# Optimization experiments

Measured on AMD Instinct MI355X. Metric: run time of the kernel, lower is better.

## Reference

```python
import jax, jax.numpy as jnp
import numpy as np

B, I, T, H, K = 64, 32, 1024, 512, 8  # K = number of extra pathways


def setup_inputs() -> dict:
    key = jax.random.key(0)
    ks = jax.random.split(key, 32)
    stdv = 1.0 / np.sqrt(H)
    u = lambda k, shp: jax.random.uniform(k, shp, jnp.float32, -stdv, stdv)
    inp = {}
    inp['Y'] = jax.random.normal(ks[0], (B, I, T), jnp.float32)
    for j in range(K):
        inp[f'x{j+1}'] = jax.random.normal(ks[1 + j], (B, 3, T), jnp.float32)
    # main gates
    inp['W_i'], inp['U_i'], inp['b_i'] = u(ks[9], (I, H)), u(ks[10], (H, H)), u(ks[11], (H,))
    inp['W_f'], inp['U_f'], inp['b_f'] = u(ks[12], (I, H)), u(ks[13], (H, H)), u(ks[14], (H,))
    inp['W_c'], inp['U_c'], inp['b_c'] = u(ks[15], (I, H)), u(ks[16], (H, H)), u(ks[17], (H,))
    inp['W_o'], inp['U_o'], inp['b_o'] = u(ks[18], (I, H)), u(ks[19], (H, H)), u(ks[20], (H,))
    # stacked extra pathways: [K,3,H], [K,H,H], [K,H]
    inp['W_i_x'] = u(ks[21], (K, 3, H))
    inp['U_i_x'] = u(ks[22], (K, H, H))
    inp['b_i_x'] = u(ks[23], (K, H))
    inp['W_c_x'] = u(ks[24], (K, 3, H))
    inp['U_c_x'] = u(ks[25], (K, H, H))
    inp['b_c_x'] = u(ks[26], (K, H))
    inp['W_a'], inp['b_a'] = u(ks[27], (H, H)), u(ks[28], (H,))
    return inp


def _forward(Y, x1, x2, x3, x4, x5, x6, x7, x8,
             W_i, U_i, b_i, W_f, U_f, b_f, W_c, U_c, b_c, W_o, U_o, b_o,
             W_i_x, U_i_x, b_i_x, W_c_x, U_c_x, b_c_x, W_a, b_a):
    xs = jnp.stack([x1, x2, x3, x4, x5, x6, x7, x8], axis=0)  # [K,B,3,T]
    # Original code quirk: input gates i_x3..i_x8 all consume x2_t.
    gate_idx = jnp.array([0, 1, 1, 1, 1, 1, 1, 1])
    xs_i = xs[gate_idx]                                        # [K,B,3,T]
    Y_T = jnp.transpose(Y, (2, 0, 1))        # [T,B,I]
    xsi_T = jnp.transpose(xs_i, (3, 1, 0, 2))  # [T,B,K,3]
    xsc_T = jnp.transpose(xs, (3, 1, 0, 2))    # [T,B,K,3]

    def step(carry, inp):
        h, c = carry
        Y_t, xi_t, xc_t = inp
        i_t = jax.nn.sigmoid(Y_t @ W_i + h @ U_i + b_i)                      # [B,H]
        i_x = jax.nn.sigmoid(jnp.einsum('bki,kih->bkh', xi_t, W_i_x)
                             + jnp.einsum('bh,kho->bko', h, U_i_x) + b_i_x)  # [B,K,H]
        f_t = jax.nn.sigmoid(Y_t @ W_f + h @ U_f + b_f)
        Ct = jnp.tanh(Y_t @ W_c + h @ U_c + b_c)
        Cx = jnp.tanh(jnp.einsum('bki,kih->bkh', xc_t, W_c_x)
                      + jnp.einsum('bh,kho->bko', h, U_c_x) + b_c_x)
        o_t = jax.nn.sigmoid(Y_t @ W_o + h @ U_o + b_o)
        l_all = jnp.concatenate([(Ct * i_t)[:, None, :], Cx * i_x], axis=1)  # [B,9,H]
        u_all = jnp.tanh(jnp.einsum('bkh,ho->bko', l_all, W_a) * c[:, None, :] + b_a)
        alpha = jax.nn.softmax(u_all, axis=1)
        L_t = jnp.sum(alpha * l_all, axis=1)                                 # [B,H]
        c = f_t * c + L_t
        h = o_t * jnp.tanh(c)
        return (h, c), h

    h0 = jnp.zeros((Y.shape[0], W_a.shape[0]), Y.dtype)
    (h_T, _), hs = jax.lax.scan(step, (h0, h0), (Y_T, xsi_T, xsc_T))
    hidden_seq = jnp.transpose(hs, (1, 0, 2))  # [B,T,H]
    return h_T, hidden_seq


def reference(Y, x1, x2, x3, x4, x5, x6, x7, x8,
              W_i, U_i, b_i, W_f, U_f, b_f, W_c, U_c, b_c, W_o, U_o, b_o,
              W_i_x, U_i_x, b_i_x, W_c_x, U_c_x, b_c_x, W_a, b_a):
    return _forward(Y, x1, x2, x3, x4, x5, x6, x7, x8,
                    W_i, U_i, b_i, W_f, U_f, b_f, W_c, U_c, b_c, W_o, U_o, b_o,
                    W_i_x, U_i_x, b_i_x, W_c_x, U_c_x, b_c_x, W_a, b_a)
```

## Files before the change

### kernel.cpp

```cpp
#include <hip/hip_runtime.h>
#include <hip/hip_bf16.h>

typedef __hip_bfloat16 bf16;
typedef unsigned long long u64;

#define NSTEP 1024
#define BATCH 64
#define HID   512
#define GRID  256
#define NTHR  512
#define KC    64

#define OFF_BAR   0u
#define OFF_FLAG  640u
#define OFF_HG    1024u
#define OFF_CG    132096u
#define OFF_GALL  263168u
#define OFF_UCAT  2884608u
#define OFF_WA    23856128u
#define OFF_WM    24904704u
#define OFF_WX    25166848u
#define OFF_BM    25265152u
#define OFF_BX    25273344u
#define OFF_BA    25306112u
#define OFF_YT    25308160u
#define OFF_XT    33696768u

#define L_US    0
#define L_WML   20960
#define L_HA    22400
#define L_YA    31104
#define L_XA    33216
#define L_RED   34752
#define L_GB    36224
#define L_LB    31104
#define L_RA    22400
#define L_RB    27264
#define L_MPZ   29696
#define L_TOT   39240

#define US(c,k)    smem[L_US  + (c)*524 + (k)]
#define WML(c,j)   smem[L_WML + (c)*36  + (j)]
#define HA(s,b,k)  smem[L_HA  + (s)*4352 + (b)*68 + (k)]
#define YA(b,j)    smem[L_YA  + (b)*33 + (j)]
#define XA(a,b,j)  smem[L_XA  + ((a)*64 + (b))*3 + (j)]
#define RED(q,j)   smem[L_RED + (q)*11 + (j)]
#define GB(r,c)    smem[L_GB  + (r)*40 + (c)]
#define LB(j,h)    smem[L_LB  + (j)*520 + (h)]

struct RawIn {
  const void *Y, *x[8];
  const void *W_i,*U_i,*b_i, *W_f,*U_f,*b_f, *W_c,*U_c,*b_c, *W_o,*U_o,*b_o;
  const void *W_ix,*U_ix,*b_ix, *W_cx,*U_cx,*b_cx, *W_a,*b_a;
  float *Ucat,*Wa,*Wm,*Wx,*Bm,*Bx,*Ba,*Yt,*Xt;
  const unsigned *flag;
};

struct Params {
  const float *Ucat,*Wa,*Wm,*Wx,*Bm,*Bx,*Ba,*Yt,*Xt;
  float *Hg,*Cg,*Gall;
  unsigned *bar;
  const unsigned *flag;
  void *out;
};

__global__ void k_detect(const unsigned short* __restrict__ p, unsigned* flag) {
  if (blockIdx.x == 0 && threadIdx.x == 0) {
    int cnt = 0;
    for (int i = 0; i < 64; ++i) {
      unsigned e = (p[i] >> 7) & 0xFF;
      cnt += (e >= 0x60 && e <= 0x7C) || (p[i] & 0x7FFF) == 0;
    }
    *flag = (cnt >= 56) ? 1u : 0u;
  }
}

__device__ __forceinline__ float cvt(const void* p, size_t i, bool bf) {
  return bf ? (float)((const bf16*)p)[i] : ((const float*)p)[i];
}

#define NWTOT 5605888
__global__ __launch_bounds__(256)
void k_conv_w(RawIn R) {
  const bool bf = (*R.flag) != 0;
  for (size_t i = blockIdx.x*256 + threadIdx.x; i < NWTOT; i += (size_t)gridDim.x*256) {
    if (i < 5242880) {
      size_t g = i >> 18, r = i & 262143;
      const void* s = g<4 ? (g==0?R.U_i:g==1?R.U_f:g==2?R.U_c:R.U_o)
                    : g<12 ? R.U_ix : R.U_cx;
      size_t off = g<4 ? r : g<12 ? (g-4)*262144 + r : (g-12)*262144 + r;
      R.Ucat[i] = cvt(s, off, bf);
    } else {
      size_t j = i - 5242880;
      if (j < 262144) { R.Wa[j] = cvt(R.W_a, j, bf); }
      else {
        size_t j2 = j - 262144;
        if (j2 < 65536) {
          size_t g = j2 >> 14, r = j2 & 16383;
          const void* s = g==0?R.W_i:g==1?R.W_f:g==2?R.W_c:R.W_o;
          R.Wm[j2] = cvt(s, r, bf);
        } else {
          size_t j3 = j2 - 65536;
          if (j3 < 24576) {
            size_t p = j3 / 1536, r = j3 % 1536;
            R.Wx[j3] = p < 8 ? cvt(R.W_ix, p*1536 + r, bf)
                             : cvt(R.W_cx, (p-8)*1536 + r, bf);
          } else {
            size_t j4 = j3 - 24576;
            if (j4 < 2048) {
              size_t g = j4 >> 9, c = j4 & 511;
              const void* s = g==0?R.b_i:g==1?R.b_f:g==2?R.b_c:R.b_o;
              R.Bm[j4] = cvt(s, c, bf);
            } else {
              size_t j5 = j4 - 2048;
              if (j5 < 8192) {
                size_t p = j5 >> 9, c = j5 & 511;
                R.Bx[j5] = p < 8 ? cvt(R.b_ix, p*512 + c, bf)
                                 : cvt(R.b_cx, (p-8)*512 + c, bf);
              } else {
                size_t j6 = j5 - 8192;
                R.Ba[j6] = cvt(R.b_a, j6, bf);
              }
            }
          }
        }
      }
    }
  }
}

#define NYT 2097152
#define NXT 1572864
__global__ __launch_bounds__(256)
void k_conv_in(RawIn R) {
  const bool bf = (*R.flag) != 0;
  for (size_t i = blockIdx.x*256 + threadIdx.x; i < NYT+NXT; i += (size_t)gridDim.x*256) {
    if (i < NYT) {
      size_t j = i & 31, b = (i >> 5) & 63, t = i >> 11;
      R.Yt[i] = cvt(R.Y, (b*32 + j)*NSTEP + t, bf);
    } else {
      size_t i2 = i - NYT;
      size_t j = i2 % 3, r = i2 / 3;
      size_t b = r & 63; r >>= 6;
      size_t a = r & 7, t = r >> 3;
      R.Xt[i2] = cvt(R.x[a], (b*3 + j)*NSTEP + t, bf);
    }
  }
}


__device__ __forceinline__ float sigf(float v){ return 1.f/(1.f+expf(-v)); }

__device__ __forceinline__ float gload(const float* p){
  return __hip_atomic_load(p, __ATOMIC_RELAXED, __HIP_MEMORY_SCOPE_AGENT);
}
__device__ __forceinline__ u64 gload2(const float* p){
  return __hip_atomic_load((const u64*)p, __ATOMIC_RELAXED, __HIP_MEMORY_SCOPE_AGENT);
}
__device__ __forceinline__ void gstore(float* p, float v){
  __hip_atomic_store(p, v, __ATOMIC_RELAXED, __HIP_MEMORY_SCOPE_AGENT);
}
__device__ __forceinline__ void gstore2(float* p, float x, float y){
  union { u64 u_; float f[2]; } v; v.f[0]=x; v.f[1]=y;
  __hip_atomic_store((u64*)p, v.u_, __ATOMIC_RELAXED, __HIP_MEMORY_SCOPE_AGENT);
}

__device__ __forceinline__ void gbar(unsigned* base, unsigned bi, int w) {
  asm volatile("s_waitcnt vmcnt(0)" ::: "memory");
  __syncthreads();
  if (threadIdx.x == 0) {
    unsigned* xcd  = base + 16 + 16*(w & 7);
    unsigned* glob = base;
    unsigned* rel  = base + 144;
    __hip_atomic_fetch_add(xcd, 1u, __ATOMIC_RELAXED, __HIP_MEMORY_SCOPE_AGENT);
    if (w < 8) {
      unsigned* mine = base + 16 + 16*w;
      while (__hip_atomic_load(mine, __ATOMIC_RELAXED, __HIP_MEMORY_SCOPE_AGENT) < bi*32u)
        __builtin_amdgcn_s_sleep(1);
      __hip_atomic_fetch_add(glob, 1u, __ATOMIC_RELAXED, __HIP_MEMORY_SCOPE_AGENT);
    }
    if (w == 0) {
      while (__hip_atomic_load(glob, __ATOMIC_RELAXED, __HIP_MEMORY_SCOPE_AGENT) < bi*8u)
        __builtin_amdgcn_s_sleep(1);
      __hip_atomic_store(rel, bi, __ATOMIC_RELAXED, __HIP_MEMORY_SCOPE_AGENT);
    } else {
      while (__hip_atomic_load(rel, __ATOMIC_RELAXED, __HIP_MEMORY_SCOPE_AGENT) < bi)
        __builtin_amdgcn_s_sleep(2);
    }
  }
  __syncthreads();
}


__global__ __launch_bounds__(NTHR, 2)
void lstm_main(Params P) {
  extern __shared__ float smem[];

  const bool bfout = (*P.flag) != 0;

  const int w   = blockIdx.x;
  const int tid = threadIdx.x;
  const int c0  = w * 40;
  const int cgr = tid & 7;
  const int rgr = (tid >> 3) & 31;
  const int ksl = tid >> 8;
  const int cl  = cgr * 5;
  const int pb  = w >> 2;
  const int ph0 = (w & 3) * 128;
  const int hg  = tid & 63;
  const int kq8 = tid >> 6;

  for (int e = tid; e < 40*512; e += NTHR) {
    int c = e >> 9, k = e & 511;
    int cg = c0 + c, g = cg >> 9, cc = cg & 511;
    US(c, k) = P.Ucat[((size_t)g*HID + k)*HID + cc];
  }
  for (int e = tid; e < 40*33; e += NTHR) {
    int c = e / 33, jj = e % 33;
    int cg = c0 + c, g = cg >> 9, cc = cg & 511;
    float v;
    if (jj == 32) {
      v = g < 4  ? P.Bm[g*HID + cc]
        : g < 12 ? P.Bx[(g-4)*HID + cc]
                 : P.Bx[(8 + g-12)*HID + cc];
    } else if (g < 4) {
      v = P.Wm[((size_t)g*32 + jj)*HID + cc];
    } else if (jj < 3) {
      int p = (g < 12) ? (g-4) : (8 + g-12);
      v = P.Wx[((size_t)p*3 + jj)*HID + cc];
    } else v = 0.f;
    WML(c, jj) = v;
  }
  __syncthreads();

  unsigned bi = 0;

  u64 pre[8];
  auto hgld = [&](int kcc) {
#pragma unroll
    for (int u = 0; u < 8; ++u) {
      int e2 = tid + u*NTHR;
      int s2 = e2 >> 11, b = (e2 >> 5) & 63, k = (e2 & 31) * 2;
      pre[u] = gload2(&P.Hg[(size_t)b*HID + s2*256 + kcc + k]);
    }
  };

  for (int t = 0; t < NSTEP; ++t) {
    for (int e = tid; e < 64*32; e += NTHR) {
      int b = e >> 5, j = e & 31;
      YA(b, j) = P.Yt[((size_t)t*BATCH + b)*32 + j];
    }
    for (int e = tid; e < 8*64*3; e += NTHR) {
      int j2 = e % 3; int r = e / 3; int b = r & 63; int a = r >> 6;
      XA(a, b, j2) = P.Xt[(((size_t)t*8 + a)*BATCH + b)*3 + j2];
    }

    hgld(0);

    float acc[2][5];
#pragma unroll
    for (int i=0;i<2;++i)
#pragma unroll
      for (int j=0;j<5;++j) acc[i][j]=0.f;

    for (int kc = 0; kc < 256; kc += KC) {
      __syncthreads();
#pragma unroll
      for (int u = 0; u < 8; ++u) {
        int e2 = tid + u*NTHR;
        int s2 = e2 >> 11, b = (e2 >> 5) & 63, k = (e2 & 31) * 2;
        union { u64 u_; float f[2]; } v; v.u_ = pre[u];
        float2 t2; t2.x = v.f[0]; t2.y = v.f[1];
        *(float2*)&HA(s2, b, k) = t2;
      }
      __syncthreads();
      if (kc + KC < 256) hgld(kc + KC);

      const int kb = ksl*256 + kc;
#pragma unroll 4
      for (int kk = 0; kk < KC; kk += 4) {
        float4 h0 = *(const float4*)&HA(ksl, rgr,      kk);
        float4 h1 = *(const float4*)&HA(ksl, rgr+32,   kk);
#pragma unroll
        for (int j = 0; j < 5; ++j) {
          float4 u = *(const float4*)&US(cl+j, kb+kk);
          acc[0][j] += h0.x*u.x; acc[0][j] += h0.y*u.y;
          acc[0][j] += h0.z*u.z; acc[0][j] += h0.w*u.w;
          acc[1][j] += h1.x*u.x; acc[1][j] += h1.y*u.y;
          acc[1][j] += h1.z*u.z; acc[1][j] += h1.w*u.w;
        }
      }
    }

    if (ksl) {
      int q = tid - 256;
#pragma unroll
      for (int i=0;i<2;++i)
#pragma unroll
        for (int j=0;j<5;++j) RED(q, i*5+j) = acc[i][j];
    }
    __syncthreads();

    float vv[2][5];
    if (!ksl) {
#pragma unroll
      for (int i = 0; i < 2; ++i) {
        int row = rgr + 32*i;
#pragma unroll
        for (int j = 0; j < 5; ++j) {
          int c = cl + j, cg = c0 + c, g = cg >> 9;
          float v = acc[i][j] + RED(tid, i*5+j);
          float s = WML(c, 32);
          if (g < 4) {
            for (int jj = 0; jj < 32; ++jj)
              s += YA(row, jj) * WML(c, jj);
            v += s;
            v = (g==2) ? tanhf(v) : sigf(v);
          } else if (g < 12) {
            int p = g-4; int a = (p==0) ? 0 : 1;
            for (int jj = 0; jj < 3; ++jj)
              s += XA(a, row, jj) * WML(c, jj);
            v = sigf(v + s);
          } else {
            int p = g-12;
            for (int jj = 0; jj < 3; ++jj)
              s += XA(p, row, jj) * WML(c, jj);
            v = tanhf(v + s);
          }
          vv[i][j] = v;
        }
      }
    }
    __syncthreads();
    if (!ksl) {
#pragma unroll
      for (int i = 0; i < 2; ++i)
#pragma unroll
        for (int j = 0; j < 5; ++j)
          GB(rgr + 32*i, cl + j) = vv[i][j];
    }
    __syncthreads();
    for (int e = tid; e < 64*20; e += NTHR) {
      int row = e / 20, p = e % 20;
      int cc2 = c0 + 2*p;
      int g = cc2 >> 9, cc = cc2 & 511;
      gstore2(&P.Gall[((size_t)g*BATCH + row)*HID + cc], GB(row, 2*p), GB(row, 2*p+1));
    }

    gbar(P.bar, ++bi, w);

    for (int e = tid; e < 9*256; e += NTHR) {
      int j = e >> 8, h2 = (e & 255) << 1;
      union { u64 u_; float f[2]; } a, b2;
      if (j == 0) {
        a.u_  = gload2(&P.Gall[((size_t)0*BATCH+pb)*HID+h2]);
        b2.u_ = gload2(&P.Gall[((size_t)2*BATCH+pb)*HID+h2]);
      } else {
        int p = j-1;
        a.u_  = gload2(&P.Gall[((size_t)(4+p)*BATCH+pb)*HID+h2]);
        b2.u_ = gload2(&P.Gall[((size_t)(12+p)*BATCH+pb)*HID+h2]);
      }
      float2 t2; t2.x = a.f[0]*b2.f[0]; t2.y = a.f[1]*b2.f[1];
      *(float2*)&LB(j, h2) = t2;
    }
    __syncthreads();

    float ab[2][9];
#pragma unroll
    for (int s=0;s<2;++s)
#pragma unroll
      for (int j=0;j<9;++j) ab[s][j]=0.f;
    {
      const int k0 = kq8 * 64;
      const float* wa = P.Wa + (size_t)k0*HID + ph0 + hg*2;
#pragma unroll 4
      for (int k = 0; k < 64; k += 4) {
        float2 w0 = *(const float2*)&wa[(size_t)(k+0)*HID];
        float2 w1 = *(const float2*)&wa[(size_t)(k+1)*HID];
        float2 w2 = *(const float2*)&wa[(size_t)(k+2)*HID];
        float2 w3 = *(const float2*)&wa[(size_t)(k+3)*HID];
#pragma unroll
        for (int j=0;j<9;++j) {
          float4 l4 = *(const float4*)&LB(j, k0+k);
          ab[0][j] += l4.x*w0.x; ab[0][j] += l4.y*w1.x;
          ab[0][j] += l4.z*w2.x; ab[0][j] += l4.w*w3.x;
          ab[1][j] += l4.x*w0.y; ab[1][j] += l4.y*w1.y;
          ab[1][j] += l4.z*w2.y; ab[1][j] += l4.w*w3.y;
        }
      }
    }
    if (tid >= 256) {
      float* r = &smem[L_RA + (tid-256)*19];
#pragma unroll
      for (int s=0;s<2;++s)
#pragma unroll
        for (int j=0;j<9;++j) r[s*9+j] = ab[s][j];
    }
    __syncthreads();
    if (tid < 256) {
      const float* r = &smem[L_RA + tid*19];
#pragma unroll
      for (int s=0;s<2;++s)
#pragma unroll
        for (int j=0;j<9;++j) ab[s][j] += r[s*9+j];
      if (tid >= 128) {
        float* r2 = &smem[L_RB + (tid-128)*19];
#pragma unroll
        for (int s=0;s<2;++s)
#pragma unroll
          for (int j=0;j<9;++j) r2[s*9+j] = ab[s][j];
      }
    }
    __syncthreads();
    if (tid < 128) {
      const float* r = &smem[L_RB + tid*19];
#pragma unroll
      for (int s=0;s<2;++s)
#pragma unroll
        for (int j=0;j<9;++j) ab[s][j] += r[s*9+j];
      if (tid >= 64) {
        float* r2 = &smem[L_RA + (tid-64)*19];
#pragma unroll
        for (int s=0;s<2;++s)
#pragma unroll
          for (int j=0;j<9;++j) r2[s*9+j] = ab[s][j];
      }
    }
    __syncthreads();
    if (tid < 64) {
      const float* r = &smem[L_RA + tid*19];
      float* mp = &smem[L_MPZ + tid*19];
#pragma unroll
      for (int s=0;s<2;++s)
#pragma unroll
        for (int j=0;j<9;++j) mp[s*9+j] = ab[s][j] + r[s*9+j];
    }
    __syncthreads();
    if (tid < 128) {
      const int hp = ph0 + tid;
      const float* mf = &smem[L_MPZ + (tid>>1)*19 + (tid&1)*9];
      float co = P.Cg[(size_t)pb*HID + hp];
      float ba = P.Ba[hp];
      float u9[9], mx = -1e30f;
#pragma unroll
      for (int j=0;j<9;++j) {
        u9[j] = tanhf(mf[j]*co + ba);
        mx = fmaxf(mx, u9[j]);
      }
      float ssum = 0.f, L = 0.f;
#pragma unroll
      for (int j=0;j<9;++j) {
        float e2 = expf(u9[j]-mx);
        ssum += e2;
        L += e2 * LB(j, hp);
      }
      L /= ssum;
      float f = gload(&P.Gall[((size_t)1*BATCH+pb)*HID + hp]);
      float o = gload(&P.Gall[((size_t)3*BATCH+pb)*HID + hp]);
      float cn = f*co + L;
      float hn = o*tanhf(cn);
      P.Cg[(size_t)pb*HID + hp] = cn;
      gstore(&P.Hg[(size_t)pb*HID + hp], hn);
      size_t iseq = (size_t)BATCH*HID + ((size_t)pb*NSTEP + t)*HID + hp;
      if (bfout) ((bf16*)P.out)[iseq] = __float2bfloat16(hn);
      else       ((float*)P.out)[iseq] = hn;
      if (t == NSTEP-1) {
        size_t ih = (size_t)pb*HID + hp;
        if (bfout) ((bf16*)P.out)[ih] = __float2bfloat16(hn);
        else       ((float*)P.out)[ih] = hn;
      }
    }

    gbar(P.bar, ++bi, w);
  }
}


extern "C" void kernel_launch(void* const* d_in, const int* in_sizes, int n_in,
                              void* d_out, int out_size, void* d_ws, size_t ws_size,
                              hipStream_t stream) {
  char* ws = (char*)d_ws;

  RawIn R;
  R.Y = d_in[0];
  for (int i = 0; i < 8; ++i) R.x[i] = d_in[1+i];
  R.W_i=d_in[9];  R.U_i=d_in[10]; R.b_i=d_in[11];
  R.W_f=d_in[12]; R.U_f=d_in[13]; R.b_f=d_in[14];
  R.W_c=d_in[15]; R.U_c=d_in[16]; R.b_c=d_in[17];
  R.W_o=d_in[18]; R.U_o=d_in[19]; R.b_o=d_in[20];
  R.W_ix=d_in[21]; R.U_ix=d_in[22]; R.b_ix=d_in[23];
  R.W_cx=d_in[24]; R.U_cx=d_in[25]; R.b_cx=d_in[26];
  R.W_a =d_in[27]; R.b_a =d_in[28];
  R.Ucat=(float*)(ws+OFF_UCAT); R.Wa=(float*)(ws+OFF_WA);
  R.Wm=(float*)(ws+OFF_WM); R.Wx=(float*)(ws+OFF_WX);
  R.Bm=(float*)(ws+OFF_BM); R.Bx=(float*)(ws+OFF_BX); R.Ba=(float*)(ws+OFF_BA);
  R.Yt=(float*)(ws+OFF_YT); R.Xt=(float*)(ws+OFF_XT);
  R.flag=(const unsigned*)(ws+OFF_FLAG);

  Params P;
  P.Ucat=R.Ucat; P.Wa=R.Wa; P.Wm=R.Wm; P.Wx=R.Wx;
  P.Bm=R.Bm; P.Bx=R.Bx; P.Ba=R.Ba; P.Yt=R.Yt; P.Xt=R.Xt;
  P.Hg=(float*)(ws+OFF_HG); P.Cg=(float*)(ws+OFF_CG); P.Gall=(float*)(ws+OFF_GALL);
  P.bar=(unsigned*)(ws+OFF_BAR);
  P.flag=R.flag;
  P.out=d_out;

  hipMemsetAsync(d_ws, 0, OFF_GALL, stream);

  k_detect<<<1, 64, 0, stream>>>((const unsigned short*)d_in[10], (unsigned*)(ws+OFF_FLAG));
  k_conv_w <<<21899, 256, 0, stream>>>(R);
  k_conv_in<<<14336, 256, 0, stream>>>(R);

  const int smemBytes = L_TOT * 4;
  hipFuncSetAttribute((const void*)lstm_main,
                      hipFuncAttributeMaxDynamicSharedMemorySize, smemBytes);
  lstm_main<<<dim3(GRID), dim3(NTHR), smemBytes, stream>>>(P);
}
```

Before: 51.85 ms.

## Split recurrent matmul into four K-slices with packed FMA and vectorized input projection

Restructures the per-step recurrent h·U product so each thread computes 4 batch rows × 5 columns over a quarter of K, instead of 2 rows over a half. The inner product uses v_pk_fma_f32 packed float2 FMAs, and the four partial sums are reduced through shared memory. The Y·W input projection is vectorized with float4 loads, with padded layouts to match. The aim is more register reuse of the U loads and higher FMA throughput per instruction. In exchange it uses more accumulator registers and adds a 4-way shared-memory reduction with an extra barrier.

```diff
diff --git a/kernel.cpp b/kernel.cpp
--- a/kernel.cpp
+++ b/kernel.cpp
@@ -9,7 +9,6 @@
 #define HID   512
 #define GRID  256
 #define NTHR  512
-#define KC    64
 
 #define OFF_BAR   0u
 #define OFF_FLAG  640u
@@ -29,22 +28,21 @@
 #define L_US    0
 #define L_WML   20960
 #define L_HA    22400
-#define L_YA    31104
-#define L_XA    33216
-#define L_RED   34752
-#define L_GB    36224
-#define L_LB    31104
+#define L_YA    31616
+#define L_XA    33920
+#define L_GB    35456
+#define L_REDA  22400
+#define L_LB    31616
 #define L_RA    22400
 #define L_RB    27264
 #define L_MPZ   29696
-#define L_TOT   39240
+#define L_TOT   38016
 
 #define US(c,k)    smem[L_US  + (c)*524 + (k)]
 #define WML(c,j)   smem[L_WML + (c)*36  + (j)]
-#define HA(s,b,k)  smem[L_HA  + (s)*4352 + (b)*68 + (k)]
-#define YA(b,j)    smem[L_YA  + (b)*33 + (j)]
+#define HA(q,b,k)  smem[L_HA  + (q)*2304 + (b)*36 + (k)]
+#define YA(b,j)    smem[L_YA  + (b)*36 + (j)]
 #define XA(a,b,j)  smem[L_XA  + ((a)*64 + (b))*3 + (j)]
-#define RED(q,j)   smem[L_RED + (q)*11 + (j)]
 #define GB(r,c)    smem[L_GB  + (r)*40 + (c)]
 #define LB(j,h)    smem[L_LB  + (j)*520 + (h)]
 
@@ -165,6 +163,10 @@
   __hip_atomic_store((u64*)p, v.u_, __ATOMIC_RELAXED, __HIP_MEMORY_SCOPE_AGENT);
 }
 
+__device__ __forceinline__ void pkfma(float2& d, float2 a, float2 b){
+  asm("v_pk_fma_f32 %0, %1, %2, %0" : "+v"(d) : "v"(a), "v"(b));
+}
+
 __device__ __forceinline__ void gbar(unsigned* base, unsigned bi, int w) {
   asm volatile("s_waitcnt vmcnt(0)" ::: "memory");
   __syncthreads();
@@ -202,8 +204,8 @@
   const int tid = threadIdx.x;
   const int c0  = w * 40;
   const int cgr = tid & 7;
-  const int rgr = (tid >> 3) & 31;
-  const int ksl = tid >> 8;
+  const int rgr = (tid >> 3) & 15;
+  const int ksl = tid >> 7;
   const int cl  = cgr * 5;
   const int pb  = w >> 2;
   const int ph0 = (w & 3) * 128;
@@ -215,20 +217,20 @@
     int cg = c0 + c, g = cg >> 9, cc = cg & 511;
     US(c, k) = P.Ucat[((size_t)g*HID + k)*HID + cc];
   }
-  for (int e = tid; e < 40*33; e += NTHR) {
-    int c = e / 33, jj = e % 33;
+  for (int e = tid; e < 40*36; e += NTHR) {
+    int c = e / 36, jj = e % 36;
     int cg = c0 + c, g = cg >> 9, cc = cg & 511;
-    float v;
+    float v = 0.f;
     if (jj == 32) {
       v = g < 4  ? P.Bm[g*HID + cc]
         : g < 12 ? P.Bx[(g-4)*HID + cc]
                  : P.Bx[(8 + g-12)*HID + cc];
-    } else if (g < 4) {
+    } else if (jj < 32 && g < 4) {
       v = P.Wm[((size_t)g*32 + jj)*HID + cc];
     } else if (jj < 3) {
       int p = (g < 12) ? (g-4) : (8 + g-12);
       v = P.Wx[((size_t)p*3 + jj)*HID + cc];
-    } else v = 0.f;
+    }
     WML(c, jj) = v;
   }
   __syncthreads();
@@ -240,8 +242,10 @@
 #pragma unroll
     for (int u = 0; u < 8; ++u) {
       int e2 = tid + u*NTHR;
-      int s2 = e2 >> 11, b = (e2 >> 5) & 63, k = (e2 & 31) * 2;
-      pre[u] = gload2(&P.Hg[(size_t)b*HID + s2*256 + kcc + k]);
+      int k  = (e2 & 15) * 2;
+      int b  = (e2 >> 4) & 63;
+      int q  = e2 >> 10;
+      pre[u] = gload2(&P.Hg[(size_t)b*HID + q*128 + kcc + k]);
     }
   };
 
@@ -257,87 +261,147 @@
 
     hgld(0);
 
-    float acc[2][5];
-#pragma unroll
-    for (int i=0;i<2;++i)
-#pragma unroll
-      for (int j=0;j<5;++j) acc[i][j]=0.f;
-
-    for (int kc = 0; kc < 256; kc += KC) {
+    float2 acc2[4][5];
+#pragma unroll
+    for (int i=0;i<4;++i)
+#pragma unroll
+      for (int j=0;j<5;++j) { acc2[i][j].x=0.f; acc2[i][j].y=0.f; }
+
+    for (int kc = 0; kc < 128; kc += 32) {
       __syncthreads();
 #pragma unroll
       for (int u = 0; u < 8; ++u) {
         int e2 = tid + u*NTHR;
-        int s2 = e2 >> 11, b = (e2 >> 5) & 63, k = (e2 & 31) * 2;
+        int k  = (e2 & 15) * 2;
+        int b  = (e2 >> 4) & 63;
+        int q  = e2 >> 10;
         union { u64 u_; float f[2]; } v; v.u_ = pre[u];
         float2 t2; t2.x = v.f[0]; t2.y = v.f[1];
-        *(float2*)&HA(s2, b, k) = t2;
+        *(float2*)&HA(q, b, k) = t2;
       }
       __syncthreads();
-      if (kc + KC < 256) hgld(kc + KC);
-
-      const int kb = ksl*256 + kc;
-#pragma unroll 4
-      for (int kk = 0; kk < KC; kk += 4) {
+      if (kc + 32 < 128) hgld(kc + 32);
+
+      const int kbase = ksl*128 + kc;
+#pragma unroll 2
+      for (int kk = 0; kk < 32; kk += 4) {
         float4 h0 = *(const float4*)&HA(ksl, rgr,      kk);
-        float4 h1 = *(const float4*)&HA(ksl, rgr+32,   kk);
+        float4 h1 = *(const float4*)&HA(ksl, rgr+16,   kk);
+        float4 h2 = *(const float4*)&HA(ksl, rgr+32,   kk);
+        float4 h3 = *(const float4*)&HA(ksl, rgr+48,   kk);
 #pragma unroll
         for (int j = 0; j < 5; ++j) {
-          float4 u = *(const float4*)&US(cl+j, kb+kk);
-          acc[0][j] += h0.x*u.x; acc[0][j] += h0.y*u.y;
-          acc[0][j] += h0.z*u.z; acc[0][j] += h0.w*u.w;
-          acc[1][j] += h1.x*u.x; acc[1][j] += h1.y*u.y;
-          acc[1][j] += h1.z*u.z; acc[1][j] += h1.w*u.w;
+          float4 uv = *(const float4*)&US(cl+j, kbase+kk);
+          float2 ulo; ulo.x = uv.x; ulo.y = uv.y;
+          float2 uhi; uhi.x = uv.z; uhi.y = uv.w;
+          float2 a0; a0.x = h0.x; a0.y = h0.y;  pkfma(acc2[0][j], a0, ulo);
+          float2 b0; b0.x = h0.z; b0.y = h0.w;  pkfma(acc2[0][j], b0, uhi);
+          float2 a1; a1.x = h1.x; a1.y = h1.y;  pkfma(acc2[1][j], a1, ulo);
+          float2 b1; b1.x = h1.z; b1.y = h1.w;  pkfma(acc2[1][j], b1, uhi);
+          float2 a2; a2.x = h2.x; a2.y = h2.y;  pkfma(acc2[2][j], a2, ulo);
+          float2 b2; b2.x = h2.z; b2.y = h2.w;  pkfma(acc2[2][j], b2, uhi);
+          float2 a3; a3.x = h3.x; a3.y = h3.y;  pkfma(acc2[3][j], a3, ulo);
+          float2 b3; b3.x = h3.z; b3.y = h3.w;  pkfma(acc2[3][j], b3, uhi);
         }
       }
     }
 
+    float accs[4][5];
+#pragma unroll
+    for (int i=0;i<4;++i)
+#pragma unroll
+      for (int j=0;j<5;++j) accs[i][j] = acc2[i][j].x + acc2[i][j].y;
+
+    __syncthreads();
     if (ksl) {
-      int q = tid - 256;
-#pragma unroll
-      for (int i=0;i<2;++i)
-#pragma unroll
-        for (int j=0;j<5;++j) RED(q, i*5+j) = acc[i][j];
-    }
-    __syncthreads();
-
-    float vv[2][5];
+      float* r = &smem[L_REDA + (tid-128)*22];
+#pragma unroll
+      for (int p=0;p<10;++p) {
+        float2 t2; t2.x = accs[(2*p)/5][(2*p)%5]; t2.y = accs[(2*p+1)/5][(2*p+1)%5];
+        *(float2*)&r[2*p] = t2;
+      }
+    }
+    __syncthreads();
     if (!ksl) {
 #pragma unroll
-      for (int i = 0; i < 2; ++i) {
-        int row = rgr + 32*i;
-#pragma unroll
+      for (int q2 = 0; q2 < 3; ++q2) {
+        const float* r = &smem[L_REDA + (tid + q2*128)*22];
+#pragma unroll
+        for (int p=0;p<10;++p) {
+          float2 t2 = *(const float2*)&r[2*p];
+          accs[(2*p)/5][(2*p)%5]   += t2.x;
+          accs[(2*p+1)/5][(2*p+1)%5] += t2.y;
+        }
+      }
+
+      const int col0 = c0 + cl;
+      const int gA = col0 >> 9, gB2 = (col0 + 4) >> 9;
+      if (gA == gB2 && gA < 4) {
+#pragma unroll
+        for (int jb = 0; jb < 8; ++jb) {
+          float4 wm0 = *(const float4*)&WML(cl+0, 4*jb);
+          float4 wm1 = *(const float4*)&WML(cl+1, 4*jb);
+          float4 wm2 = *(const float4*)&WML(cl+2, 4*jb);
+          float4 wm3 = *(const float4*)&WML(cl+3, 4*jb);
+          float4 wm4 = *(const float4*)&WML(cl+4, 4*jb);
+#pragma unroll
+          for (int i=0;i<4;++i) {
+            float4 ya = *(const float4*)&YA(rgr+16*i, 4*jb);
+            accs[i][0] += ya.x*wm0.x + ya.y*wm0.y + ya.z*wm0.z + ya.w*wm0.w;
+            accs[i][1] += ya.x*wm1.x + ya.y*wm1.y + ya.z*wm1.z + ya.w*wm1.w;
+            accs[i][2] += ya.x*wm2.x + ya.y*wm2.y + ya.z*wm2.z + ya.w*wm2.w;
+            accs[i][3] += ya.x*wm3.x + ya.y*wm3.y + ya.z*wm3.z + ya.w*wm3.w;
+            accs[i][4] += ya.x*wm4.x + ya.y*wm4.y + ya.z*wm4.z + ya.w*wm4.w;
+          }
+        }
+#pragma unroll
+        for (int i=0;i<4;++i)
+#pragma unroll
+          for (int j=0;j<5;++j) {
+            float v = accs[i][j] + WML(cl+j, 32);
+            v = (gA == 2) ? tanhf(v) : sigf(v);
+            GB(rgr + 16*i, cl+j) = v;
+          }
+      } else {
         for (int j = 0; j < 5; ++j) {
           int c = cl + j, cg = c0 + c, g = cg >> 9;
-          float v = acc[i][j] + RED(tid, i*5+j);
-          float s = WML(c, 32);
           if (g < 4) {
-            for (int jj = 0; jj < 32; ++jj)
-              s += YA(row, jj) * WML(c, jj);
-            v += s;
-            v = (g==2) ? tanhf(v) : sigf(v);
+#pragma unroll
+            for (int i=0;i<4;++i) {
+              int row = rgr + 16*i;
+              float s = WML(c, 32);
+#pragma unroll
+              for (int jb = 0; jb < 8; ++jb) {
+                float4 ya = *(const float4*)&YA(row, 4*jb);
+                float4 wm = *(const float4*)&WML(c, 4*jb);
+                s += ya.x*wm.x + ya.y*wm.y + ya.z*wm.z + ya.w*wm.w;
+              }
+              float v = accs[i][j] + s;
+              GB(row, c) = (g == 2) ? tanhf(v) : sigf(v);
+            }
           } else if (g < 12) {
             int p = g-4; int a = (p==0) ? 0 : 1;
-            for (int jj = 0; jj < 3; ++jj)
-              s += XA(a, row, jj) * WML(c, jj);
-            v = sigf(v + s);
+#pragma unroll
+            for (int i=0;i<4;++i) {
+              int row = rgr + 16*i;
+              float s = WML(c, 32);
+              for (int jj = 0; jj < 3; ++jj)
+                s += XA(a, row, jj) * WML(c, jj);
+              GB(row, c) = sigf(accs[i][j] + s);
+            }
           } else {
             int p = g-12;
-            for (int jj = 0; jj < 3; ++jj)
-              s += XA(p, row, jj) * WML(c, jj);
-            v = tanhf(v + s);
+#pragma unroll
+            for (int i=0;i<4;++i) {
+              int row = rgr + 16*i;
+              float s = WML(c, 32);
+              for (int jj = 0; jj < 3; ++jj)
+                s += XA(p, row, jj) * WML(c, jj);
+              GB(row, c) = tanhf(accs[i][j] + s);
+            }
           }
-          vv[i][j] = v;
         }
       }
-    }
-    __syncthreads();
-    if (!ksl) {
-#pragma unroll
-      for (int i = 0; i < 2; ++i)
-#pragma unroll
-        for (int j = 0; j < 5; ++j)
-          GB(rgr + 32*i, cl + j) = vv[i][j];
     }
     __syncthreads();
     for (int e = tid; e < 64*20; e += NTHR) {
```

Result: slower. 125.0 ms (+141.0%).
